# Performance work log

Hardware: AMD Instinct MI355X
Metric: run time of the kernel (lower is better)

The kernel has to match this reference:

```python
import jax, jax.numpy as jnp
import numpy as np

EPS = 1e-8

def _cosine_sim(a, b):
    # a: [B,Nq,D], b: [B,Np,D] -> [B,Nq,Np]
    an = a / (jnp.linalg.norm(a, axis=-1, keepdims=True) + EPS)
    bn = b / (jnp.linalg.norm(b, axis=-1, keepdims=True) + EPS)
    return jnp.einsum('bqd,bpd->bqp', an, bn)

def _sq_dist(a, b):
    # squared euclidean pairwise distance: [B,Nq,Np]
    d = (jnp.sum(a * a, -1)[:, :, None] + jnp.sum(b * b, -1)[:, None, :]
         - 2.0 * jnp.einsum('bqd,bpd->bqp', a, b))
    return jnp.maximum(d, 0.0)

def setup_inputs() -> dict:
    key = jax.random.key(0)
    ks = jax.random.split(key, 6)
    B, N, D, H = 8, 2048, 256, 16
    return {
        'f1': jax.random.normal(ks[0], (B, N, D), jnp.float32),
        'f2': jax.random.normal(ks[1], (B, N, D), jnp.float32),
        'p': jax.random.normal(ks[2], (B, N, 3), jnp.float32),
        'q': jax.random.normal(ks[3], (B, N, 3), jnp.float32),
        'W1': jax.random.normal(ks[4], (H, 2), jnp.float32) * 0.5,
        'b1': jnp.zeros((H,), jnp.float32),
        'W2': jax.random.normal(ks[5], (1, H), jnp.float32) * 0.5,
        'b2': jnp.zeros((1,), jnp.float32),
        'similar_num': 8,
    }

def reference(f1, f2, p, q, W1, b1, W2, b2, similar_num):
    B, Nq, _ = q.shape
    Np = p.shape[1]
    # pairwise similarities
    w1 = _cosine_sim(f2, f1)            # [B,Nq,Np] feature cosine sim
    w2 = -_sq_dist(q, p)                # [B,Nq,Np] negative coord distance
    # similar_net: pointwise MLP over channel dim (2 -> H -> 1)
    w_in = jnp.stack([w1.reshape(B, -1), w2.reshape(B, -1)], axis=1)  # [B,2,L]
    h = jax.nn.relu(jnp.einsum('bcl,hc->bhl', w_in, W1) + b1[None, :, None])
    w = (jnp.einsum('bhl,oh->bol', h, W2) + b2[None, :, None]).reshape(B, Nq, Np)
    # get_weighted_similarity: topk + softmax-weighted pooling + max pooling
    vals, idx = jax.lax.top_k(w, similar_num)          # [B,Nq,k] (sorted desc, as torch.topk)
    ws = jax.nn.softmax(vals, axis=-1)                 # softmax over gathered scores
    feat = jax.vmap(lambda z, i: z[i])(f1, idx)        # [B,Nq,k,D] gather
    feat_max = jnp.max(feat, axis=2)                   # [B,Nq,D]
    feat_w = jnp.einsum('bqk,bqkd->bqd', ws, feat)     # [B,Nq,D]
    f = jnp.concatenate([feat_w, feat_max], axis=-1)   # [B,Nq,2D]
    return f, idx, w
```

## Files before the change

kernel.cpp:

```cpp
#include <hip/hip_runtime.h>
#include <math.h>

constexpr int B_ = 8;
constexpr int N_ = 2048;
constexpr int D_ = 256;
constexpr int H_ = 16;
constexpr int K_ = 8;
constexpr int CAND = 32;

constexpr int BM = 128;
constexpr int BK = 32;

typedef _Float16 f16x8 __attribute__((ext_vector_type(8)));
typedef float    f32x4 __attribute__((ext_vector_type(4)));
typedef float    f32x2 __attribute__((ext_vector_type(2)));

typedef __attribute__((address_space(3))) unsigned int       lds_u32_t;
typedef __attribute__((address_space(1))) const unsigned int glb_u32_t;

__device__ __forceinline__ void g2l16(const void* g, void* l) {
    __builtin_amdgcn_global_load_lds((glb_u32_t*)g, (lds_u32_t*)l, 16, 0, 0);
}

__device__ __forceinline__ unsigned ford(float f) {
    unsigned u = __float_as_uint(f);
    return (u & 0x80000000u) ? ~u : (u | 0x80000000u);
}

__device__ __forceinline__ unsigned pk16(_Float16 a, _Float16 b) {
    unsigned short ua = __builtin_bit_cast(unsigned short, a);
    unsigned short ub = __builtin_bit_cast(unsigned short, b);
    return (unsigned)ua | ((unsigned)ub << 16);
}

__device__ inline void split4_f16(float4 v, float s, uint2& hi, uint2& lo) {
    float a = v.x * s, b = v.y * s, c = v.z * s, d = v.w * s;
    _Float16 ha = (_Float16)a, hb = (_Float16)b;
    _Float16 hc = (_Float16)c, hd = (_Float16)d;
    _Float16 la = (_Float16)(a - (float)ha), lb = (_Float16)(b - (float)hb);
    _Float16 lc = (_Float16)(c - (float)hc), ld = (_Float16)(d - (float)hd);
    hi.x = pk16(ha, hb); hi.y = pk16(hc, hd);
    lo.x = pk16(la, lb); lo.y = pk16(lc, ld);
}

__global__ __launch_bounds__(256)
void prep_kernel(const float* __restrict__ f1, const float* __restrict__ f2,
                 unsigned short* __restrict__ s1h, unsigned short* __restrict__ s1l,
                 unsigned short* __restrict__ s2h) {
    int gid  = blockIdx.x * blockDim.x + threadIdx.x;
    int wave = gid >> 6;
    int lane = gid & 63;
    if (wave >= 2 * B_ * N_) return;
    bool is1 = wave < B_ * N_;
    int r = is1 ? wave : wave - B_ * N_;

    const float* src = (is1 ? f1 : f2) + (size_t)r * D_;
    float4 v = *(const float4*)(src + lane * 4);
    float ss = v.x * v.x + v.y * v.y + v.z * v.z + v.w * v.w;
#pragma unroll
    for (int off = 32; off > 0; off >>= 1) ss += __shfl_xor(ss, off, 64);
    float inv = 1.0f / (sqrtf(ss) + 1e-8f);

    uint2 hi, lo;
    split4_f16(v, inv, hi, lo);

    int panel = r >> 7, rloc = r & 127;
    int s     = lane >> 1;
    int chunk = s >> 2;
    int sl    = (s & 3) ^ ((rloc >> 1) & 3);
    int half  = lane & 1;
    size_t idx = ((size_t)(panel * 8 + chunk) << 12)
               + (size_t)rloc * 32 + sl * 8 + half * 4;
    if (is1) {
        *(uint2*)&s1h[idx] = hi;
        *(uint2*)&s1l[idx] = lo;
    } else {
        *(uint2*)&s2h[idx] = hi;
    }
}

__global__ __launch_bounds__(256, 3)
void gemm_mlp_kernel(const unsigned short* __restrict__ aH0,
                     const unsigned short* __restrict__ bH0,
                     const unsigned short* __restrict__ bL0,
                     const float* __restrict__ pc, const float* __restrict__ qc,
                     const float* __restrict__ pW1, const float* __restrict__ pb1,
                     const float* __restrict__ pW2, const float* __restrict__ pb2,
                     float* __restrict__ w_out) {
    __shared__ unsigned short ldsbuf[2 * 3 * 4096];

    int tid = threadIdx.x;
    int l  = blockIdx.x + (blockIdx.y << 4);
    int ls = ((l & 7) << 5) | (l >> 3);
    int pBase = (ls & 15) * BM;
    int qBase = (ls >> 4) * BM;
    int b = blockIdx.z;

    int lane = tid & 63;
    int wv   = tid >> 6;
    int wq = (wv >> 1) * 64;
    int wp = (wv & 1) * 64;
    int fr = lane & 15;
    int kg = lane >> 4;

    const int Apanel8 = ((b * N_ + qBase) >> 7) * 8;
    const int Bpanel8 = ((b * N_ + pBase) >> 7) * 8;

    char* ldsB = (char*)&ldsbuf[0];
    const int wlo = (wv << 11) + (lane << 4);
    const int wdo = (wv << 11);
    const int cw  = (kg ^ ((fr >> 1) & 3)) << 4;

    f32x4 acc[4][4] = {};

#define STAGE(buf, c)                                                          \
    {                                                                          \
        const char* aH = (const char*)aH0 + ((size_t)(Apanel8 + (c)) << 13);   \
        const char* bH = (const char*)bH0 + ((size_t)(Bpanel8 + (c)) << 13);   \
        const char* bL = (const char*)bL0 + ((size_t)(Bpanel8 + (c)) << 13);   \
        char* dst = ldsB + (buf) * 24576;                                      \
        _Pragma("unroll")                                                      \
        for (int i = 0; i < 2; i++) {                                          \
            int o = i << 10;                                                   \
            g2l16(aH + wlo + o, dst + 0     + wdo + o);                        \
            g2l16(bH + wlo + o, dst + 8192  + wdo + o);                        \
            g2l16(bL + wlo + o, dst + 16384 + wdo + o);                        \
        }                                                                      \
    }

    STAGE(0, 0);
    __syncthreads();

#pragma unroll
    for (int c = 0; c < 8; c++) {
        if (c < 7) STAGE((c + 1) & 1, c + 1);

        char* base = ldsB + (c & 1) * 24576;
        f16x8 ah[4], bh[4], bl[4];
#pragma unroll
        for (int t = 0; t < 4; t++) {
            int ra = (wq + t * 16 + fr) * 64;
            int rb = (wp + t * 16 + fr) * 64;
            ah[t] = *(const f16x8*)(base + 0     + ra + cw);
            bh[t] = *(const f16x8*)(base + 8192  + rb + cw);
            bl[t] = *(const f16x8*)(base + 16384 + rb + cw);
        }
#pragma unroll
        for (int qt = 0; qt < 4; qt++) {
#pragma unroll
            for (int pt = 0; pt < 4; pt++) {
                acc[qt][pt] = __builtin_amdgcn_mfma_f32_16x16x32_f16(
                    ah[qt], bh[pt], acc[qt][pt], 0, 0, 0);
                acc[qt][pt] = __builtin_amdgcn_mfma_f32_16x16x32_f16(
                    ah[qt], bl[pt], acc[qt][pt], 0, 0, 0);
            }
        }
        __syncthreads();
    }
#undef STAGE

    float Wa[H_], Wb[H_], Bb[H_], Wo[H_];
#pragma unroll
    for (int h = 0; h < H_; h++) {
        Wa[h] = pW1[2 * h]; Wb[h] = pW1[2 * h + 1];
        Bb[h] = pb1[h];     Wo[h] = pW2[h];
    }
    float base2 = pb2[0];

    float px[4], py[4], pz[4], pn2[4];
    int pg[4];
#pragma unroll
    for (int pt = 0; pt < 4; pt++) {
        int p = pBase + wp + pt * 16 + fr;
        pg[pt] = p;
        const float* pp = pc + ((size_t)(b * N_ + p)) * 3;
        px[pt] = pp[0]; py[pt] = pp[1]; pz[pt] = pp[2];
        pn2[pt] = px[pt] * px[pt] + py[pt] * py[pt] + pz[pt] * pz[pt];
    }
#pragma unroll
    for (int qt = 0; qt < 4; qt++) {
        float qx[4], qy[4], qz[4], qq2[4];
        int q0 = qBase + wq + qt * 16 + kg * 4;
#pragma unroll
        for (int r = 0; r < 4; r++) {
            const float* qp = qc + ((size_t)(b * N_ + q0 + r)) * 3;
            qx[r] = qp[0]; qy[r] = qp[1]; qz[r] = qp[2];
            qq2[r] = qx[r] * qx[r] + qy[r] * qy[r] + qz[r] * qz[r];
        }
#pragma unroll
        for (int pt = 0; pt < 4; pt++) {
            f32x4 cval = acc[qt][pt];
            float w2v[4];
#pragma unroll
            for (int r = 0; r < 4; r++) {
                float d2 = qq2[r] + pn2[pt]
                         - 2.f * (qx[r] * px[pt] + qy[r] * py[pt] + qz[r] * pz[pt]);
                w2v[r] = -fmaxf(d2, 0.f);
            }
#pragma unroll
            for (int pr = 0; pr < 2; pr++) {
                f32x2 w1p = { cval[2 * pr], cval[2 * pr + 1] };
                f32x2 w2p = { w2v[2 * pr], w2v[2 * pr + 1] };
                f32x2 outp = { base2, base2 };
#pragma unroll
                for (int h = 0; h < H_; h++) {
                    f32x2 t = w1p * Wa[h] + w2p * Wb[h] + Bb[h];
                    t = __builtin_elementwise_max(t, (f32x2){0.f, 0.f});
                    outp += Wo[h] * t;
                }
                w_out[((size_t)(b * N_ + q0 + 2 * pr)) * N_ + pg[pt]]     = outp.x;
                w_out[((size_t)(b * N_ + q0 + 2 * pr + 1)) * N_ + pg[pt]] = outp.y;
            }
        }
    }
}

__global__ __launch_bounds__(256)
void topk_kernel(const float* __restrict__ w, const float* __restrict__ f1,
                 const float* __restrict__ f2,
                 const float* __restrict__ pc, const float* __restrict__ qc,
                 const float* __restrict__ pW1, const float* __restrict__ pb1,
                 const float* __restrict__ pW2, const float* __restrict__ pb2,
                 float* __restrict__ f_out, float* __restrict__ idx_out) {
    __shared__ int    s_cand[4][CAND];
    __shared__ double s_val[4][CAND];
    __shared__ int    s_idx[4][CAND];
    __shared__ double s_rv[4][K_];
    __shared__ int    s_ri[4][K_];

    int tid  = threadIdx.x;
    int wix  = tid >> 6;
    int lane = tid & 63;
    int row  = blockIdx.x * 4 + wix;
    int b    = row >> 11;
    const float* wrow = w + (size_t)row * N_;

    float tv[K_];
    int   ti[K_];
#pragma unroll
    for (int s = 0; s < K_; s++) { tv[s] = -INFINITY; ti[s] = 0x7fffffff; }
    for (int j = 0; j < N_ / 256; j++) {
        float4 v4 = *(const float4*)(wrow + lane * 4 + j * 256);
        float vv[4] = {v4.x, v4.y, v4.z, v4.w};
#pragma unroll
        for (int c = 0; c < 4; c++) {
            float v = vv[c];
            if (v > tv[K_ - 1]) {
                int idx = lane * 4 + j * 256 + c;
                tv[K_ - 1] = v; ti[K_ - 1] = idx;
#pragma unroll
                for (int s = K_ - 1; s > 0; s--) {
                    if (tv[s] > tv[s - 1]) {
                        float tf = tv[s]; tv[s] = tv[s - 1]; tv[s - 1] = tf;
                        int tn = ti[s]; ti[s] = ti[s - 1]; ti[s - 1] = tn;
                    }
                }
            }
        }
    }

    unsigned uk[K_];
#pragma unroll
    for (int s = 0; s < K_; s++) uk[s] = ford(tv[s]);

    unsigned T = 0;
    for (int bit = 31; bit >= 0; --bit) {
        unsigned c = T | (1u << bit);
        int cnt = 0;
#pragma unroll
        for (int s = 0; s < K_; s++)
            cnt += __popcll(__ballot(uk[s] >= c));
        if (cnt >= CAND) T = c;
    }
    unsigned long long below = (1ull << lane) - 1ull;
    int total = 0;
#pragma unroll
    for (int s = 0; s < K_; s++) {
        unsigned long long m = __ballot(uk[s] >= T);
        int pos = total + __popcll(m & below);
        if (uk[s] >= T && pos < CAND) s_cand[wix][pos] = ti[s];
        total += __popcll(m);
    }
    __syncthreads();

    int sl = lane & 7;
    int gr = lane >> 3;
    const float* f2r = f2 + (size_t)row * D_ + sl * 32;
    float4 a4[8];
#pragma unroll
    for (int t = 0; t < 8; t++) a4[t] = *(const float4*)(f2r + t * 4);

    double daa = 0.0;
#pragma unroll
    for (int t = 0; t < 8; t++) {
        daa += (double)a4[t].x * (double)a4[t].x;
        daa += (double)a4[t].y * (double)a4[t].y;
        daa += (double)a4[t].z * (double)a4[t].z;
        daa += (double)a4[t].w * (double)a4[t].w;
    }
#pragma unroll
    for (int off = 1; off < 8; off <<= 1) daa += __shfl_xor(daa, off, 64);
    double inv_a = 1.0 / (sqrt(daa) + 1e-8);

    double mydab = 0.0, mydbb = 0.0;
    int myci = 0x7fffffff;
#pragma unroll
    for (int r = 0; r < 4; r++) {
        int cj = s_cand[wix][8 * r + gr];
        const float* f1r = f1 + ((size_t)(b * N_ + cj)) * D_ + sl * 32;
        double sA = 0.0, sB = 0.0;
#pragma unroll
        for (int t = 0; t < 8; t++) {
            float4 b4 = *(const float4*)(f1r + t * 4);
            double b0 = b4.x, b1 = b4.y, b2 = b4.z, b3 = b4.w;
            sA += (double)a4[t].x * b0; sB += b0 * b0;
            sA += (double)a4[t].y * b1; sB += b1 * b1;
            sA += (double)a4[t].z * b2; sB += b2 * b2;
            sA += (double)a4[t].w * b3; sB += b3 * b3;
        }
#pragma unroll
        for (int off = 1; off < 8; off <<= 1) {
            sA += __shfl_xor(sA, off, 64);
            sB += __shfl_xor(sB, off, 64);
        }
        if (sl == r) { mydab = sA; mydbb = sB; myci = cj; }
    }

    double ex = -INFINITY;
    int    ei = 0x7fffffff;
    if (sl < 4) {
        ei = myci;
        double w1d = mydab * inv_a * (1.0 / (sqrt(mydbb) + 1e-8));
        const float* qp = qc + (size_t)row * 3;
        double qx = qp[0], qy = qp[1], qz = qp[2];
        const float* pp = pc + ((size_t)(b * N_ + myci)) * 3;
        double px = pp[0], py = pp[1], pz = pp[2];
        double d2 = (qx * qx + qy * qy + qz * qz) + (px * px + py * py + pz * pz)
                  - 2.0 * (qx * px + qy * py + qz * pz);
        double w2d = -fmax(d2, 0.0);
        double out = (double)pb2[0];
#pragma unroll
        for (int h = 0; h < H_; h++) {
            double t = (double)pW1[2 * h] * w1d + (double)pW1[2 * h + 1] * w2d
                     + (double)pb1[h];
            out += (double)pW2[h] * fmax(t, 0.0);
        }
        ex = out;
    }

    int slot = gr * 4 + sl;
    if (sl < 4) {
        s_val[wix][slot] = ex;
        s_idx[wix][slot] = ei;
    }
    asm volatile("s_waitcnt lgkmcnt(0)" ::: "memory");
    if (sl < 4) {
        int rank = 0;
#pragma unroll
        for (int j = 0; j < CAND; j++) {
            double vj = s_val[wix][j];
            int    ij = s_idx[wix][j];
            rank += (vj > ex || (vj == ex && ij < ei)) ? 1 : 0;
        }
        if (rank < K_) { s_rv[wix][rank] = ex; s_ri[wix][rank] = ei; }
    }
    asm volatile("s_waitcnt lgkmcnt(0)" ::: "memory");

    double outv[K_];
    int    outi[K_];
#pragma unroll
    for (int r = 0; r < K_; r++) { outv[r] = s_rv[wix][r]; outi[r] = s_ri[wix][r]; }

    float m = (float)outv[0];
    float e[K_], s = 0.f;
#pragma unroll
    for (int r = 0; r < K_; r++) { e[r] = expf((float)outv[r] - m); s += e[r]; }
    float inv_s = 1.f / s;

    const float* f1b = f1 + ((size_t)b * N_) * D_;
    size_t obase = (size_t)row * (2 * D_);
#pragma unroll
    for (int jd = 0; jd < D_ / 64; jd++) {
        int d = lane + 64 * jd;
        float accv = 0.f, mx = -INFINITY;
#pragma unroll
        for (int r = 0; r < K_; r++) {
            float x = f1b[(size_t)outi[r] * D_ + d];
            accv += (e[r] * inv_s) * x;
            mx = fmaxf(mx, x);
        }
        f_out[obase + d]      = accv;
        f_out[obase + D_ + d] = mx;
    }
    if (lane == 0) {
#pragma unroll
        for (int r = 0; r < K_; r++) idx_out[(size_t)row * K_ + r] = (float)outi[r];
    }
}

extern "C" void kernel_launch(void* const* d_in, const int* in_sizes, int n_in,
                              void* d_out, int out_size, void* d_ws, size_t ws_size,
                              hipStream_t stream) {
    const float* f1 = (const float*)d_in[0];
    const float* f2 = (const float*)d_in[1];
    const float* pc = (const float*)d_in[2];
    const float* qc = (const float*)d_in[3];
    const float* W1 = (const float*)d_in[4];
    const float* b1 = (const float*)d_in[5];
    const float* W2 = (const float*)d_in[6];
    const float* b2 = (const float*)d_in[7];

    float* out     = (float*)d_out;
    float* f_out   = out;
    float* idx_out = f_out + (size_t)B_ * N_ * 2 * D_;
    float* w_out   = idx_out + (size_t)B_ * N_ * K_;

    unsigned short* s1h = (unsigned short*)f_out;
    unsigned short* s1l = s1h + (size_t)B_ * N_ * D_;
    unsigned short* s2h = s1l + (size_t)B_ * N_ * D_;

    prep_kernel<<<(2 * B_ * N_) / 4, 256, 0, stream>>>(f1, f2, s1h, s1l, s2h);

    dim3 g2(N_ / BM, N_ / BM, B_);
    gemm_mlp_kernel<<<g2, 256, 0, stream>>>(s2h, s1h, s1l, pc, qc,
                                            W1, b1, W2, b2, w_out);

    topk_kernel<<<(B_ * N_) / 4, 256, 0, stream>>>(w_out, f1, f2, pc, qc,
                                                   W1, b1, W2, b2,
                                                   f_out, idx_out);
}
```

Measured before the change: 414.5 us.

## Replace per-lane top-8 insertion sort with max-threshold candidate pool and precomputed norms

The topk kernel drops the per-lane sorted top-8 insertion, which branches heavily. Each lane now takes the max of its 32 values, and a radix-style ballot search finds a threshold met by 24 lane maxima. Every value at or above that threshold is collected into a pool of up to 64 candidates, which are then rescored in double precision. The inverse norms of f1 rows are computed once in double in prep_kernel and stored in workspace, so per-candidate norm accumulation is gone. In exchange the number of rescoring iterations varies, the cap of 64 could drop true top-8 entries when many values tie, and the rank loop now runs over all 64 slots.

```diff
diff --git a/kernel.cpp b/kernel.cpp
--- a/kernel.cpp
+++ b/kernel.cpp
@@ -6,7 +6,8 @@
 constexpr int D_ = 256;
 constexpr int H_ = 16;
 constexpr int K_ = 8;
-constexpr int CAND = 32;
+constexpr int POOL = 64;
+constexpr int PSEL = 24;
 
 constexpr int BM = 128;
 constexpr int BK = 32;
@@ -25,6 +26,10 @@
 __device__ __forceinline__ unsigned ford(float f) {
     unsigned u = __float_as_uint(f);
     return (u & 0x80000000u) ? ~u : (u | 0x80000000u);
+}
+__device__ __forceinline__ float unford(unsigned t) {
+    return (t & 0x80000000u) ? __uint_as_float(t & 0x7FFFFFFFu)
+                             : __uint_as_float(~t);
 }
 
 __device__ __forceinline__ unsigned pk16(_Float16 a, _Float16 b) {
@@ -46,7 +51,7 @@
 __global__ __launch_bounds__(256)
 void prep_kernel(const float* __restrict__ f1, const float* __restrict__ f2,
                  unsigned short* __restrict__ s1h, unsigned short* __restrict__ s1l,
-                 unsigned short* __restrict__ s2h) {
+                 unsigned short* __restrict__ s2h, double* __restrict__ dinv1) {
     int gid  = blockIdx.x * blockDim.x + threadIdx.x;
     int wave = gid >> 6;
     int lane = gid & 63;
@@ -74,6 +79,11 @@
     if (is1) {
         *(uint2*)&s1h[idx] = hi;
         *(uint2*)&s1l[idx] = lo;
+        double dss = (double)v.x * v.x + (double)v.y * v.y
+                   + (double)v.z * v.z + (double)v.w * v.w;
+#pragma unroll
+        for (int off = 32; off > 0; off >>= 1) dss += __shfl_xor(dss, off, 64);
+        if (lane == 0) dinv1[r] = 1.0 / (sqrt(dss) + 1e-8);
     } else {
         *(uint2*)&s2h[idx] = hi;
     }
@@ -221,10 +231,11 @@
                  const float* __restrict__ pc, const float* __restrict__ qc,
                  const float* __restrict__ pW1, const float* __restrict__ pb1,
                  const float* __restrict__ pW2, const float* __restrict__ pb2,
+                 const double* __restrict__ dinv1,
                  float* __restrict__ f_out, float* __restrict__ idx_out) {
-    __shared__ int    s_cand[4][CAND];
-    __shared__ double s_val[4][CAND];
-    __shared__ int    s_idx[4][CAND];
+    __shared__ int    s_cand[4][POOL];
+    __shared__ double s_val[4][POOL];
+    __shared__ int    s_idx[4][POOL];
     __shared__ double s_rv[4][K_];
     __shared__ int    s_ri[4][K_];
 
@@ -235,53 +246,41 @@
     int b    = row >> 11;
     const float* wrow = w + (size_t)row * N_;
 
-    float tv[K_];
-    int   ti[K_];
-#pragma unroll
-    for (int s = 0; s < K_; s++) { tv[s] = -INFINITY; ti[s] = 0x7fffffff; }
-    for (int j = 0; j < N_ / 256; j++) {
-        float4 v4 = *(const float4*)(wrow + lane * 4 + j * 256);
-        float vv[4] = {v4.x, v4.y, v4.z, v4.w};
-#pragma unroll
-        for (int c = 0; c < 4; c++) {
-            float v = vv[c];
-            if (v > tv[K_ - 1]) {
-                int idx = lane * 4 + j * 256 + c;
-                tv[K_ - 1] = v; ti[K_ - 1] = idx;
-#pragma unroll
-                for (int s = K_ - 1; s > 0; s--) {
-                    if (tv[s] > tv[s - 1]) {
-                        float tf = tv[s]; tv[s] = tv[s - 1]; tv[s - 1] = tf;
-                        int tn = ti[s]; ti[s] = ti[s - 1]; ti[s - 1] = tn;
-                    }
-                }
-            }
-        }
-    }
-
-    unsigned uk[K_];
-#pragma unroll
-    for (int s = 0; s < K_; s++) uk[s] = ford(tv[s]);
-
+    float4 v4s[8];
+    float mymax = -INFINITY;
+#pragma unroll
+    for (int j = 0; j < 8; j++) {
+        v4s[j] = *(const float4*)(wrow + lane * 4 + j * 256);
+        mymax = fmaxf(mymax,
+                 fmaxf(fmaxf(v4s[j].x, v4s[j].y), fmaxf(v4s[j].z, v4s[j].w)));
+    }
+
+    unsigned mk = ford(mymax);
     unsigned T = 0;
     for (int bit = 31; bit >= 0; --bit) {
         unsigned c = T | (1u << bit);
-        int cnt = 0;
-#pragma unroll
-        for (int s = 0; s < K_; s++)
-            cnt += __popcll(__ballot(uk[s] >= c));
-        if (cnt >= CAND) T = c;
-    }
+        if (__popcll(__ballot(mk >= c)) >= PSEL) T = c;
+    }
+    float Tf = unford(T);
+
     unsigned long long below = (1ull << lane) - 1ull;
     int total = 0;
 #pragma unroll
-    for (int s = 0; s < K_; s++) {
-        unsigned long long m = __ballot(uk[s] >= T);
-        int pos = total + __popcll(m & below);
-        if (uk[s] >= T && pos < CAND) s_cand[wix][pos] = ti[s];
-        total += __popcll(m);
-    }
-    __syncthreads();
+    for (int j = 0; j < 8; j++) {
+        float vv[4] = {v4s[j].x, v4s[j].y, v4s[j].z, v4s[j].w};
+#pragma unroll
+        for (int c = 0; c < 4; c++) {
+            bool in = vv[c] >= Tf;
+            unsigned long long m = __ballot(in);
+            if (in) {
+                int pos = total + __popcll(m & below);
+                if (pos < POOL) s_cand[wix][pos] = lane * 4 + j * 256 + c;
+            }
+            total += __popcll(m);
+        }
+    }
+    int ncand = total < POOL ? total : POOL;
+    asm volatile("s_waitcnt lgkmcnt(0)" ::: "memory");
 
     int sl = lane & 7;
     int gr = lane >> 3;
@@ -302,35 +301,33 @@
     for (int off = 1; off < 8; off <<= 1) daa += __shfl_xor(daa, off, 64);
     double inv_a = 1.0 / (sqrt(daa) + 1e-8);
 
-    double mydab = 0.0, mydbb = 0.0;
-    int myci = 0x7fffffff;
-#pragma unroll
-    for (int r = 0; r < 4; r++) {
-        int cj = s_cand[wix][8 * r + gr];
+    double mydab = 0.0;
+    int myci = 0;
+    int NR = (ncand + 7) >> 3;
+    for (int r = 0; r < NR; r++) {
+        int k = 8 * r + gr;
+        int cj = (k < ncand) ? s_cand[wix][k] : 0;
         const float* f1r = f1 + ((size_t)(b * N_ + cj)) * D_ + sl * 32;
-        double sA = 0.0, sB = 0.0;
+        double sA = 0.0;
 #pragma unroll
         for (int t = 0; t < 8; t++) {
             float4 b4 = *(const float4*)(f1r + t * 4);
-            double b0 = b4.x, b1 = b4.y, b2 = b4.z, b3 = b4.w;
-            sA += (double)a4[t].x * b0; sB += b0 * b0;
-            sA += (double)a4[t].y * b1; sB += b1 * b1;
-            sA += (double)a4[t].z * b2; sB += b2 * b2;
-            sA += (double)a4[t].w * b3; sB += b3 * b3;
-        }
-#pragma unroll
-        for (int off = 1; off < 8; off <<= 1) {
-            sA += __shfl_xor(sA, off, 64);
-            sB += __shfl_xor(sB, off, 64);
-        }
-        if (sl == r) { mydab = sA; mydbb = sB; myci = cj; }
-    }
-
+            sA += (double)a4[t].x * (double)b4.x;
+            sA += (double)a4[t].y * (double)b4.y;
+            sA += (double)a4[t].z * (double)b4.z;
+            sA += (double)a4[t].w * (double)b4.w;
+        }
+#pragma unroll
+        for (int off = 1; off < 8; off <<= 1) sA += __shfl_xor(sA, off, 64);
+        if (sl == r) { mydab = sA; myci = cj; }
+    }
+
+    int myk = 8 * sl + gr;
     double ex = -INFINITY;
     int    ei = 0x7fffffff;
-    if (sl < 4) {
+    if (myk < ncand) {
         ei = myci;
-        double w1d = mydab * inv_a * (1.0 / (sqrt(mydbb) + 1e-8));
+        double w1d = mydab * inv_a * dinv1[b * N_ + myci];
         const float* qp = qc + (size_t)row * 3;
         double qx = qp[0], qy = qp[1], qz = qp[2];
         const float* pp = pc + ((size_t)(b * N_ + myci)) * 3;
@@ -348,16 +345,13 @@
         ex = out;
     }
 
-    int slot = gr * 4 + sl;
-    if (sl < 4) {
-        s_val[wix][slot] = ex;
-        s_idx[wix][slot] = ei;
-    }
+    s_val[wix][myk] = ex;
+    s_idx[wix][myk] = ei;
     asm volatile("s_waitcnt lgkmcnt(0)" ::: "memory");
-    if (sl < 4) {
+    {
         int rank = 0;
 #pragma unroll
-        for (int j = 0; j < CAND; j++) {
+        for (int j = 0; j < POOL; j++) {
             double vj = s_val[wix][j];
             int    ij = s_idx[wix][j];
             rank += (vj > ex || (vj == ex && ij < ei)) ? 1 : 0;
@@ -419,13 +413,16 @@
     unsigned short* s1l = s1h + (size_t)B_ * N_ * D_;
     unsigned short* s2h = s1l + (size_t)B_ * N_ * D_;
 
-    prep_kernel<<<(2 * B_ * N_) / 4, 256, 0, stream>>>(f1, f2, s1h, s1l, s2h);
+    double* dinv1 = (double*)d_ws;
+
+    prep_kernel<<<(2 * B_ * N_) / 4, 256, 0, stream>>>(f1, f2, s1h, s1l, s2h,
+                                                       dinv1);
 
     dim3 g2(N_ / BM, N_ / BM, B_);
     gemm_mlp_kernel<<<g2, 256, 0, stream>>>(s2h, s1h, s1l, pc, qc,
                                             W1, b1, W2, b2, w_out);
 
     topk_kernel<<<(B_ * N_) / 4, 256, 0, stream>>>(w_out, f1, f2, pc, qc,
-                                                   W1, b1, W2, b2,
+                                                   W1, b1, W2, b2, dinv1,
                                                    f_out, idx_out);
 }
```

Measured after the change: 388.3 us. -6.3%, faster.
